# Performance work log

Measured on AMD Instinct MI355X. Metric: run time of the kernel, lower is better.

Reference implementation:

```python
import jax, jax.numpy as jnp
import numpy as np

N_NODES = 100000
N_EDGES = 3200000
N_GRAPHS = 128
IN_DIM = 4
HID = 64
BN_EPS = 1e-5


def setup_inputs() -> dict:
    key = jax.random.key(0)
    ks = jax.random.split(key, 24)
    x = jax.random.normal(ks[0], (N_NODES, IN_DIM), dtype=jnp.float32)
    edge_index = jax.random.randint(ks[1], (2, N_EDGES), 0, N_NODES, dtype=jnp.int32)
    batch_ids = jnp.sort(jax.random.randint(ks[2], (N_NODES,), 0, N_GRAPHS, dtype=jnp.int32))

    def lin(k, out_d, in_d):
        s = 1.0 / np.sqrt(in_d)
        return jax.random.uniform(k, (out_d, in_d), jnp.float32, -s, s)

    inp = {
        'x': x, 'edge_index': edge_index, 'batch_ids': batch_ids,
        # SAGEConv i: out = lin_l(mean_neighbors) + lin_r(x_self); bias lives in lin_l
        'w1l': lin(ks[3], HID, IN_DIM), 'b1': jnp.zeros((HID,), jnp.float32), 'w1r': lin(ks[4], HID, IN_DIM),
        'bn1_g': jnp.ones((HID,), jnp.float32), 'bn1_b': jnp.zeros((HID,), jnp.float32),
        'w2l': lin(ks[5], HID, HID), 'b2': jnp.zeros((HID,), jnp.float32), 'w2r': lin(ks[6], HID, HID),
        'bn2_g': jnp.ones((HID,), jnp.float32), 'bn2_b': jnp.zeros((HID,), jnp.float32),
        'w3l': lin(ks[7], HID, HID), 'b3': jnp.zeros((HID,), jnp.float32), 'w3r': lin(ks[8], HID, HID),
        'bn3_g': jnp.ones((HID,), jnp.float32), 'bn3_b': jnp.zeros((HID,), jnp.float32),
        'fc1_w': lin(ks[9], 64, HID), 'fc1_b': jnp.zeros((64,), jnp.float32),
        'fc2_w': lin(ks[10], 2, 64), 'fc2_b': jnp.zeros((2,), jnp.float32),
    }
    return inp


def _sage(x, src, dst, deg_inv, wl, bl, wr):
    # mean-aggregate neighbor messages (source -> target), then two small GEMMs
    msum = jax.ops.segment_sum(x[src], dst, num_segments=N_NODES)  # [N, d]
    agg = msum * deg_inv[:, None]
    return agg @ wl.T + bl + x @ wr.T


def _bn(x, g, b):
    # BatchNorm1d in training mode: batch stats over node dim, biased variance
    m = jnp.mean(x, axis=0)
    v = jnp.mean((x - m) ** 2, axis=0)
    return (x - m) * jax.lax.rsqrt(v + BN_EPS) * g + b


def reference(x, edge_index, batch_ids,
              w1l, b1, w1r, bn1_g, bn1_b,
              w2l, b2, w2r, bn2_g, bn2_b,
              w3l, b3, w3r, bn3_g, bn3_b,
              fc1_w, fc1_b, fc2_w, fc2_b):
    src, dst = edge_index[0], edge_index[1]
    deg = jax.ops.segment_sum(jnp.ones((src.shape[0],), x.dtype), dst, num_segments=N_NODES)
    deg_inv = 1.0 / jnp.maximum(deg, 1.0)

    h = jax.nn.relu(_bn(_sage(x, src, dst, deg_inv, w1l, b1, w1r), bn1_g, bn1_b))
    h = jax.nn.relu(_bn(_sage(h, src, dst, deg_inv, w2l, b2, w2r), bn2_g, bn2_b))
    h = jax.nn.relu(_bn(_sage(h, src, dst, deg_inv, w3l, b3, w3r), bn3_g, bn3_b))

    # global_mean_pool over graphs
    gsum = jax.ops.segment_sum(h, batch_ids, num_segments=N_GRAPHS)
    gcnt = jax.ops.segment_sum(jnp.ones((h.shape[0],), h.dtype), batch_ids, num_segments=N_GRAPHS)
    pooled = gsum / jnp.maximum(gcnt, 1.0)[:, None]

    # MLP head (dropout = identity at inference)
    hid = jax.nn.relu(pooled @ fc1_w.T + fc1_b)
    return hid @ fc2_w.T + fc2_b
```

## Files before the change

### kernel.cpp

```cpp
#include <hip/hip_runtime.h>
#include <hip/hip_fp16.h>

#define NN 100000
#define NE 3200000
#define NG 128
#define BN_EPS 1e-5f

#define NBUK 782
#define BSHIFT 7
#define BCAP 6144

#define GRID_L1 2048
#define GRID_SG 1024
#define PBMAX 2048

typedef _Float16 h2v __attribute__((ext_vector_type(2)));

__global__ void __launch_bounds__(512) k_scatter(
    const int* __restrict__ src, const int* __restrict__ dst,
    int* __restrict__ slab_cursor, unsigned int* __restrict__ slab, int E) {
    __shared__ int hist[NBUK + 2];
    __shared__ int cbase[NBUK + 2];
    int tid = threadIdx.x;
    int eBeg = blockIdx.x * 6250;
    int eEnd = min(eBeg + 6250, E);

    for (int t = tid; t < NBUK; t += 512) hist[t] = 0;
    __syncthreads();
    for (int e = eBeg + tid; e < eEnd; e += 512) {
        int b = dst[e] >> BSHIFT;
        atomicAdd(&hist[b], 1);
    }
    __syncthreads();
    for (int t = tid; t < NBUK; t += 512) {
        int c = hist[t];
        cbase[t] = (c > 0) ? atomicAdd(&slab_cursor[t], c) : 0;
    }
    __syncthreads();
    for (int t = tid; t < NBUK; t += 512) hist[t] = 0;
    __syncthreads();
    for (int e = eBeg + tid; e < eEnd; e += 512) {
        int d = dst[e];
        int b = d >> BSHIFT;
        int r = atomicAdd(&hist[b], 1);
        int pos = cbase[b] + r;
        if (pos < BCAP) slab[(size_t)b * BCAP + pos] = ((unsigned)src[e] << BSHIFT) | (unsigned)(d & 127);
    }
}

__global__ void k_bucket_scan(const int* __restrict__ slab_cursor,
                              int* __restrict__ bucket_base, int* __restrict__ row_ptr) {
    __shared__ int sm[1024];
    int t = threadIdx.x;
    int c = (t < NBUK) ? min(slab_cursor[t], BCAP) : 0;
    sm[t] = c;
    __syncthreads();
    for (int off = 1; off < 1024; off <<= 1) {
        int add = (t >= off) ? sm[t - off] : 0;
        __syncthreads();
        sm[t] += add;
        __syncthreads();
    }
    if (t < NBUK) {
        bucket_base[t] = sm[t] - c;
        if (t == NBUK - 1) row_ptr[NN] = sm[t];
    }
}

__global__ void __launch_bounds__(512) k_bucket_csr(
    const unsigned int* __restrict__ slab, const int* __restrict__ slab_cursor,
    const int* __restrict__ bucket_base, int* __restrict__ row_ptr,
    float* __restrict__ deg_inv, int* __restrict__ csr_src) {
    __shared__ int sdeg[128];
    __shared__ int sscan[128];
    __shared__ int slcur[128];
    int tid = threadIdx.x;
    int b = blockIdx.x;
    int lo = b << BSHIFT;
    int cnt = min(slab_cursor[b], BCAP);
    const unsigned int* sl = slab + (size_t)b * BCAP;

    if (tid < 128) sdeg[tid] = 0;
    __syncthreads();
    for (int k = tid; k < cnt; k += 512) {
        atomicAdd(&sdeg[sl[k] & 127], 1);
    }
    __syncthreads();
    int v = (tid < 128) ? sdeg[tid] : 0;
    if (tid < 128) sscan[tid] = v;
    __syncthreads();
    for (int off = 1; off < 128; off <<= 1) {
        int add = 0;
        if (tid < 128 && tid >= off) add = sscan[tid - off];
        __syncthreads();
        if (tid < 128) sscan[tid] += add;
        __syncthreads();
    }
    int base = bucket_base[b];
    if (tid < 128) {
        int excl = sscan[tid] - v;
        int n = lo + tid;
        if (n < NN) {
            row_ptr[n] = base + excl;
            deg_inv[n] = 1.0f / fmaxf((float)v, 1.0f);
        }
        slcur[tid] = base + excl;
    }
    __syncthreads();
    for (int k = tid; k < cnt; k += 512) {
        unsigned int p = sl[k];
        int pos = atomicAdd(&slcur[p & 127], 1);
        csr_src[pos] = (int)(p >> BSHIFT);
    }
}

__global__ void __launch_bounds__(256) k_layer1(
    const float* __restrict__ x, const int* __restrict__ row_ptr,
    const int* __restrict__ csr_src, const float* __restrict__ deg_inv,
    const float* __restrict__ w1l, const float* __restrict__ b1,
    const float* __restrict__ w1r, float* __restrict__ h_pre,
    float* __restrict__ part, int N) {
    __shared__ float swl[256], swr[256], sb1[64];
    __shared__ float ssum[64], ssq[64];
    int tid = threadIdx.x;
    swl[tid] = w1l[tid];
    swr[tid] = w1r[tid];
    if (tid < 64) { sb1[tid] = b1[tid]; ssum[tid] = 0.f; ssq[tid] = 0.f; }
    __syncthreads();

    int g = tid & 15, ni = tid >> 4;
    const int ntiles = N / 16;

    for (int tile = blockIdx.x; tile < ntiles; tile += gridDim.x) {
        int n = tile * 16 + ni;
        int r0 = row_ptr[n], r1 = row_ptr[n + 1];
        float4 acc = make_float4(0.f, 0.f, 0.f, 0.f);
        for (int e = r0 + g; e < r1; e += 16) {
            int s = csr_src[e];
            float4 xv = ((const float4*)x)[s];
            acc.x += xv.x; acc.y += xv.y; acc.z += xv.z; acc.w += xv.w;
        }
        for (int m = 1; m < 16; m <<= 1) {
            acc.x += __shfl_xor(acc.x, m);
            acc.y += __shfl_xor(acc.y, m);
            acc.z += __shfl_xor(acc.z, m);
            acc.w += __shfl_xor(acc.w, m);
        }
        float di = deg_inv[n];
        float ax = acc.x * di, ay = acc.y * di, az = acc.z * di, aw = acc.w * di;
        float4 xs = ((const float4*)x)[n];

        float4 o;
        float* op = &o.x;
#pragma unroll
        for (int m = 0; m < 4; m++) {
            int j = 4 * g + m;
            float s = sb1[j];
            s += ax * swl[j * 4 + 0] + ay * swl[j * 4 + 1] + az * swl[j * 4 + 2] + aw * swl[j * 4 + 3];
            s += xs.x * swr[j * 4 + 0] + xs.y * swr[j * 4 + 1] + xs.z * swr[j * 4 + 2] + xs.w * swr[j * 4 + 3];
            op[m] = s;
        }
        ((float4*)h_pre)[n * 16 + g] = o;

        float4 q = make_float4(o.x * o.x, o.y * o.y, o.z * o.z, o.w * o.w);
#pragma unroll
        for (int m = 16; m <= 32; m <<= 1) {
            o.x += __shfl_xor(o.x, m); o.y += __shfl_xor(o.y, m);
            o.z += __shfl_xor(o.z, m); o.w += __shfl_xor(o.w, m);
            q.x += __shfl_xor(q.x, m); q.y += __shfl_xor(q.y, m);
            q.z += __shfl_xor(q.z, m); q.w += __shfl_xor(q.w, m);
        }
        if ((tid & 48) == 0) {
            atomicAdd(&ssum[4 * g + 0], o.x); atomicAdd(&ssum[4 * g + 1], o.y);
            atomicAdd(&ssum[4 * g + 2], o.z); atomicAdd(&ssum[4 * g + 3], o.w);
            atomicAdd(&ssq[4 * g + 0], q.x);  atomicAdd(&ssq[4 * g + 1], q.y);
            atomicAdd(&ssq[4 * g + 2], q.z);  atomicAdd(&ssq[4 * g + 3], q.w);
        }
    }
    __syncthreads();
    if (tid < 64) {
        part[(2 * tid) * PBMAX + blockIdx.x]     = ssum[tid];
        part[(2 * tid + 1) * PBMAX + blockIdx.x] = ssq[tid];
    }
}

__global__ void __launch_bounds__(512, 8) k_sage(
    const __half* __restrict__ h_in, const int* __restrict__ row_ptr,
    const int* __restrict__ csr_src, const float* __restrict__ deg_inv,
    const float* __restrict__ wl, const float* __restrict__ bl,
    const float* __restrict__ wr, float* __restrict__ h_pre,
    float* __restrict__ part) {
    __shared__ h2v wl2s[32][68];
    __shared__ h2v wr2s[32][68];
    __shared__ h2v tAh[32][36];
    __shared__ h2v tXh[32][36];
    __shared__ float ssum[64], ssq[64];
    int tid = threadIdx.x;
    for (int idx = tid; idx < 2048; idx += 512) {
        int j = idx & 63, kk = idx >> 6;
        float2 l = ((const float2*)wl)[j * 32 + kk];
        float2 r = ((const float2*)wr)[j * 32 + kk];
        wl2s[kk][j] = h2v{(_Float16)l.x, (_Float16)l.y};
        wr2s[kk][j] = h2v{(_Float16)r.x, (_Float16)r.y};
    }
    if (tid < 64) { ssum[tid] = 0.f; ssq[tid] = 0.f; }
    __syncthreads();

    int g = tid & 15, ni = tid >> 4;
    const uint2* tbl = (const uint2*)h_in;
    const int ntiles = NN / 32;

    for (int tile = blockIdx.x; tile < ntiles; tile += gridDim.x) {
        int n = tile * 32 + ni;
        float ax = 0.f, ay = 0.f, az = 0.f, aw = 0.f;
        int r0 = row_ptr[n], r1 = row_ptr[n + 1];
        int e = r0;
        for (; e + 4 <= r1; e += 4) {
            int s0 = csr_src[e], s1 = csr_src[e + 1], s2 = csr_src[e + 2], s3 = csr_src[e + 3];
            uint2 v0 = tbl[(size_t)s0 * 16 + g];
            uint2 v1 = tbl[(size_t)s1 * 16 + g];
            uint2 v2 = tbl[(size_t)s2 * 16 + g];
            uint2 v3 = tbl[(size_t)s3 * 16 + g];
            float2 f;
            f = __half22float2(*(__half2*)&v0.x); ax += f.x; ay += f.y;
            f = __half22float2(*(__half2*)&v0.y); az += f.x; aw += f.y;
            f = __half22float2(*(__half2*)&v1.x); ax += f.x; ay += f.y;
            f = __half22float2(*(__half2*)&v1.y); az += f.x; aw += f.y;
            f = __half22float2(*(__half2*)&v2.x); ax += f.x; ay += f.y;
            f = __half22float2(*(__half2*)&v2.y); az += f.x; aw += f.y;
            f = __half22float2(*(__half2*)&v3.x); ax += f.x; ay += f.y;
            f = __half22float2(*(__half2*)&v3.y); az += f.x; aw += f.y;
        }
        for (; e < r1; ++e) {
            int s = csr_src[e];
            uint2 v = tbl[(size_t)s * 16 + g];
            float2 f;
            f = __half22float2(*(__half2*)&v.x); ax += f.x; ay += f.y;
            f = __half22float2(*(__half2*)&v.y); az += f.x; aw += f.y;
        }
        float di = deg_inv[n];
        uint2 rs = tbl[(size_t)n * 16 + g];
        ax *= di; ay *= di; az *= di; aw *= di;
        tAh[ni][2 * g]     = h2v{(_Float16)ax, (_Float16)ay};
        tAh[ni][2 * g + 1] = h2v{(_Float16)az, (_Float16)aw};
        *(uint2*)&tXh[ni][2 * g] = rs;
        __syncthreads();

        float4 o = ((const float4*)bl)[g];
#pragma unroll 4
        for (int kk = 0; kk < 32; kk++) {
            h2v a2 = tAh[ni][kk];
            h2v x2 = tXh[ni][kk];
            h2v l0 = wl2s[kk][4 * g + 0], l1 = wl2s[kk][4 * g + 1];
            h2v l2 = wl2s[kk][4 * g + 2], l3 = wl2s[kk][4 * g + 3];
            h2v r0v = wr2s[kk][4 * g + 0], r1v = wr2s[kk][4 * g + 1];
            h2v r2v = wr2s[kk][4 * g + 2], r3v = wr2s[kk][4 * g + 3];
#if __has_builtin(__builtin_amdgcn_fdot2)
            o.x = __builtin_amdgcn_fdot2(a2, l0, o.x, false);
            o.y = __builtin_amdgcn_fdot2(a2, l1, o.y, false);
            o.z = __builtin_amdgcn_fdot2(a2, l2, o.z, false);
            o.w = __builtin_amdgcn_fdot2(a2, l3, o.w, false);
            o.x = __builtin_amdgcn_fdot2(x2, r0v, o.x, false);
            o.y = __builtin_amdgcn_fdot2(x2, r1v, o.y, false);
            o.z = __builtin_amdgcn_fdot2(x2, r2v, o.z, false);
            o.w = __builtin_amdgcn_fdot2(x2, r3v, o.w, false);
#else
            float a0 = (float)a2.x, a1 = (float)a2.y, x0 = (float)x2.x, x1 = (float)x2.y;
            o.x += a0 * (float)l0.x + a1 * (float)l0.y + x0 * (float)r0v.x + x1 * (float)r0v.y;
            o.y += a0 * (float)l1.x + a1 * (float)l1.y + x0 * (float)r1v.x + x1 * (float)r1v.y;
            o.z += a0 * (float)l2.x + a1 * (float)l2.y + x0 * (float)r2v.x + x1 * (float)r2v.y;
            o.w += a0 * (float)l3.x + a1 * (float)l3.y + x0 * (float)r3v.x + x1 * (float)r3v.y;
#endif
        }
        ((float4*)h_pre)[(size_t)n * 16 + g] = o;

        float4 q = make_float4(o.x * o.x, o.y * o.y, o.z * o.z, o.w * o.w);
#pragma unroll
        for (int m = 16; m <= 32; m <<= 1) {
            o.x += __shfl_xor(o.x, m); o.y += __shfl_xor(o.y, m);
            o.z += __shfl_xor(o.z, m); o.w += __shfl_xor(o.w, m);
            q.x += __shfl_xor(q.x, m); q.y += __shfl_xor(q.y, m);
            q.z += __shfl_xor(q.z, m); q.w += __shfl_xor(q.w, m);
        }
        if ((tid & 48) == 0) {
            atomicAdd(&ssum[4 * g + 0], o.x); atomicAdd(&ssum[4 * g + 1], o.y);
            atomicAdd(&ssum[4 * g + 2], o.z); atomicAdd(&ssum[4 * g + 3], o.w);
            atomicAdd(&ssq[4 * g + 0], q.x);  atomicAdd(&ssq[4 * g + 1], q.y);
            atomicAdd(&ssq[4 * g + 2], q.z);  atomicAdd(&ssq[4 * g + 3], q.w);
        }
        __syncthreads();
    }
    if (tid < 64) {
        part[(2 * tid) * PBMAX + blockIdx.x]     = ssum[tid];
        part[(2 * tid + 1) * PBMAX + blockIdx.x] = ssq[tid];
    }
}

__global__ void k_reduce_sb(const float* __restrict__ part, int PB,
                            const float* __restrict__ gamma, const float* __restrict__ beta,
                            float* __restrict__ sbv, int N) {
    int c = blockIdx.x;
    float s = 0.f, q = 0.f;
    for (int b = threadIdx.x; b < PB; b += 256) {
        s += part[(2 * c) * PBMAX + b];
        q += part[(2 * c + 1) * PBMAX + b];
    }
    __shared__ float rs[256], rq[256];
    rs[threadIdx.x] = s;
    rq[threadIdx.x] = q;
    __syncthreads();
    for (int off = 128; off > 0; off >>= 1) {
        if (threadIdx.x < off) {
            rs[threadIdx.x] += rs[threadIdx.x + off];
            rq[threadIdx.x] += rq[threadIdx.x + off];
        }
        __syncthreads();
    }
    if (threadIdx.x == 0) {
        float m = rs[0] / (float)N;
        float var = rq[0] / (float)N - m * m;
        float sc = gamma[c] * rsqrtf(var + BN_EPS);
        sbv[c]      = sc;
        sbv[64 + c] = beta[c] - m * sc;
    }
}

__global__ void k_bnrelu_h(const float* __restrict__ h_pre, const float* __restrict__ sbv,
                           __half* __restrict__ h, int N) {
    __shared__ float s_sc[64], s_bi[64];
    if (threadIdx.x < 64) {
        s_sc[threadIdx.x] = sbv[threadIdx.x];
        s_bi[threadIdx.x] = sbv[64 + threadIdx.x];
    }
    __syncthreads();
    int total = N * 16;
    for (int i = blockIdx.x * blockDim.x + threadIdx.x; i < total; i += gridDim.x * blockDim.x) {
        float4 v = ((const float4*)h_pre)[i];
        int c4 = (i & 15) * 4;
        v.x = fmaxf(v.x * s_sc[c4 + 0] + s_bi[c4 + 0], 0.f);
        v.y = fmaxf(v.y * s_sc[c4 + 1] + s_bi[c4 + 1], 0.f);
        v.z = fmaxf(v.z * s_sc[c4 + 2] + s_bi[c4 + 2], 0.f);
        v.w = fmaxf(v.w * s_sc[c4 + 3] + s_bi[c4 + 3], 0.f);
        __half2 p0 = __floats2half2_rn(v.x, v.y);
        __half2 p1 = __floats2half2_rn(v.z, v.w);
        uint2 o;
        o.x = *(unsigned int*)&p0;
        o.y = *(unsigned int*)&p1;
        ((uint2*)h)[i] = o;
    }
}

__global__ void k_poolhead(const __half* __restrict__ h, const int* __restrict__ batch,
                           const float* __restrict__ fc1w, const float* __restrict__ fc1b,
                           const float* __restrict__ fc2w, const float* __restrict__ fc2b,
                           float* __restrict__ out, int N) {
    int gph = blockIdx.x;
    int lo = 0, hi = N;
    while (lo < hi) { int mid = (lo + hi) >> 1; if (batch[mid] < gph) lo = mid + 1; else hi = mid; }
    int start = lo;
    hi = N;
    while (lo < hi) { int mid = (lo + hi) >> 1; if (batch[mid] < gph + 1) lo = mid + 1; else hi = mid; }
    int end = lo;

    int c = threadIdx.x & 63, w = threadIdx.x >> 6;
    float s = 0.f;
    for (int r = start + w; r < end; r += 4) s += __half2float(h[r * 64 + c]);
    __shared__ float sm[256];
    __shared__ float pl[64], hid[64];
    sm[threadIdx.x] = s;
    __syncthreads();
    if (threadIdx.x < 64) {
        float t = sm[c] + sm[64 + c] + sm[128 + c] + sm[192 + c];
        pl[c] = t / fmaxf((float)(end - start), 1.0f);
    }
    __syncthreads();
    if (threadIdx.x < 64) {
        int j = threadIdx.x;
        float v = fc1b[j];
        for (int k = 0; k < 64; k++) v += pl[k] * fc1w[j * 64 + k];
        hid[j] = fmaxf(v, 0.f);
    }
    __syncthreads();
    if (threadIdx.x < 2) {
        int j = threadIdx.x;
        float o = fc2b[j];
        for (int k = 0; k < 64; k++) o += hid[k] * fc2w[j * 64 + k];
        out[gph * 2 + j] = o;
    }
}

extern "C" void kernel_launch(void* const* d_in, const int* in_sizes, int n_in,
                              void* d_out, int out_size, void* d_ws, size_t ws_size,
                              hipStream_t stream) {
    const float* x    = (const float*)d_in[0];
    const int* ei     = (const int*)d_in[1];
    const int* batch  = (const int*)d_in[2];
    const float* w1l  = (const float*)d_in[3];
    const float* b1   = (const float*)d_in[4];
    const float* w1r  = (const float*)d_in[5];
    const float* bn1g = (const float*)d_in[6];
    const float* bn1b = (const float*)d_in[7];
    const float* w2l  = (const float*)d_in[8];
    const float* b2   = (const float*)d_in[9];
    const float* w2r  = (const float*)d_in[10];
    const float* bn2g = (const float*)d_in[11];
    const float* bn2b = (const float*)d_in[12];
    const float* w3l  = (const float*)d_in[13];
    const float* b3   = (const float*)d_in[14];
    const float* w3r  = (const float*)d_in[15];
    const float* bn3g = (const float*)d_in[16];
    const float* bn3b = (const float*)d_in[17];
    const float* fc1w = (const float*)d_in[18];
    const float* fc1b = (const float*)d_in[19];
    const float* fc2w = (const float*)d_in[20];
    const float* fc2b = (const float*)d_in[21];
    float* out = (float*)d_out;

    const int N = NN, E = NE;
    const int* srcp = ei;
    const int* dstp = ei + E;

    char* ws = (char*)d_ws;
    size_t off = 0;
    auto alloc = [&](size_t bytes) -> char* {
        char* p = ws + off;
        off += (bytes + 255) & ~(size_t)255;
        return p;
    };
    int* csr_src       = (int*)alloc(sizeof(int) * E);
    float* hB          = (float*)alloc(sizeof(float) * N * 64);
    __half* hH         = (__half*)alloc(sizeof(__half) * N * 64);
    unsigned int* slab = (unsigned int*)alloc(sizeof(unsigned int) * (size_t)NBUK * BCAP);
    int* slab_cursor   = (int*)alloc(sizeof(int) * NBUK);
    int* bucket_base   = (int*)alloc(sizeof(int) * NBUK);
    int* row_ptr       = (int*)alloc(sizeof(int) * (N + 1));
    float* deg_inv     = (float*)alloc(sizeof(float) * N);
    float* part        = (float*)alloc(sizeof(float) * 128 * PBMAX);
    float* sbv         = (float*)alloc(sizeof(float) * 128);

    hipMemsetAsync(slab_cursor, 0, sizeof(int) * NBUK, stream);

    k_scatter<<<512, 512, 0, stream>>>(srcp, dstp, slab_cursor, slab, E);
    k_bucket_scan<<<1, 1024, 0, stream>>>(slab_cursor, bucket_base, row_ptr);
    k_bucket_csr<<<NBUK, 512, 0, stream>>>(slab, slab_cursor, bucket_base, row_ptr, deg_inv, csr_src);

    k_layer1<<<GRID_L1, 256, 0, stream>>>(x, row_ptr, csr_src, deg_inv, w1l, b1, w1r, hB, part, N);
    k_reduce_sb<<<64, 256, 0, stream>>>(part, GRID_L1, bn1g, bn1b, sbv, N);
    k_bnrelu_h<<<1024, 256, 0, stream>>>(hB, sbv, hH, N);

    k_sage<<<GRID_SG, 512, 0, stream>>>(hH, row_ptr, csr_src, deg_inv, w2l, b2, w2r, hB, part);
    k_reduce_sb<<<64, 256, 0, stream>>>(part, GRID_SG, bn2g, bn2b, sbv, N);
    k_bnrelu_h<<<1024, 256, 0, stream>>>(hB, sbv, hH, N);

    k_sage<<<GRID_SG, 512, 0, stream>>>(hH, row_ptr, csr_src, deg_inv, w3l, b3, w3r, hB, part);
    k_reduce_sb<<<64, 256, 0, stream>>>(part, GRID_SG, bn3g, bn3b, sbv, N);
    k_bnrelu_h<<<1024, 256, 0, stream>>>(hB, sbv, hH, N);

    k_poolhead<<<NG, 256, 0, stream>>>(hH, batch, fc1w, fc1b, fc2w, fc2b, out, N);
}
```

Before: 469.3 us.

## Fuse layer-1 SAGE into CSR build and chunk fp16 features by column group

Layer 1's aggregation and linear transform now run inside the bucket CSR kernel. The kernel stages the bucket's CSR in LDS and gathers x directly, so the separate k_layer1 pass and its reread of csr_src go away. The fp16 hidden-feature table changes from row-major 128-byte rows to four column chunks of 32 bytes per node. k_sage then processes one chunk at a time, splitting edges across 4 lanes, to improve cache locality of the random gathers. The costs are more LDS use in the CSR kernel, extra shuffles and passes over csr_src in k_sage, and a matching change to the pooling and BN layouts.

```diff
diff --git a/kernel.cpp b/kernel.cpp
--- a/kernel.cpp
+++ b/kernel.cpp
@@ -10,9 +10,10 @@
 #define BSHIFT 7
 #define BCAP 6144
 
-#define GRID_L1 2048
 #define GRID_SG 1024
 #define PBMAX 2048
+
+#define CHUNK_U2 (NN * 4)
 
 typedef _Float16 h2v __attribute__((ext_vector_type(2)));
 
@@ -70,16 +71,24 @@
 __global__ void __launch_bounds__(512) k_bucket_csr(
     const unsigned int* __restrict__ slab, const int* __restrict__ slab_cursor,
     const int* __restrict__ bucket_base, int* __restrict__ row_ptr,
-    float* __restrict__ deg_inv, int* __restrict__ csr_src) {
+    float* __restrict__ deg_inv, int* __restrict__ csr_src,
+    const float* __restrict__ x, const float* __restrict__ w1l,
+    const float* __restrict__ b1, const float* __restrict__ w1r,
+    float* __restrict__ h_pre, float* __restrict__ part) {
+    __shared__ int lds_csr[BCAP];
     __shared__ int sdeg[128];
     __shared__ int sscan[128];
     __shared__ int slcur[128];
+    __shared__ float swl[256], swr[256], sb1[64];
+    __shared__ float ssum[64], ssq[64];
     int tid = threadIdx.x;
     int b = blockIdx.x;
     int lo = b << BSHIFT;
     int cnt = min(slab_cursor[b], BCAP);
     const unsigned int* sl = slab + (size_t)b * BCAP;
 
+    if (tid < 256) { swl[tid] = w1l[tid]; swr[tid] = w1r[tid]; }
+    if (tid < 64)  { sb1[tid] = b1[tid]; ssum[tid] = 0.f; ssq[tid] = 0.f; }
     if (tid < 128) sdeg[tid] = 0;
     __syncthreads();
     for (int k = tid; k < cnt; k += 512) {
@@ -104,77 +113,69 @@
             row_ptr[n] = base + excl;
             deg_inv[n] = 1.0f / fmaxf((float)v, 1.0f);
         }
-        slcur[tid] = base + excl;
+        slcur[tid] = excl;
     }
     __syncthreads();
     for (int k = tid; k < cnt; k += 512) {
         unsigned int p = sl[k];
         int pos = atomicAdd(&slcur[p & 127], 1);
-        csr_src[pos] = (int)(p >> BSHIFT);
-    }
-}
-
-__global__ void __launch_bounds__(256) k_layer1(
-    const float* __restrict__ x, const int* __restrict__ row_ptr,
-    const int* __restrict__ csr_src, const float* __restrict__ deg_inv,
-    const float* __restrict__ w1l, const float* __restrict__ b1,
-    const float* __restrict__ w1r, float* __restrict__ h_pre,
-    float* __restrict__ part, int N) {
-    __shared__ float swl[256], swr[256], sb1[64];
-    __shared__ float ssum[64], ssq[64];
-    int tid = threadIdx.x;
-    swl[tid] = w1l[tid];
-    swr[tid] = w1r[tid];
-    if (tid < 64) { sb1[tid] = b1[tid]; ssum[tid] = 0.f; ssq[tid] = 0.f; }
-    __syncthreads();
-
-    int g = tid & 15, ni = tid >> 4;
-    const int ntiles = N / 16;
-
-    for (int tile = blockIdx.x; tile < ntiles; tile += gridDim.x) {
-        int n = tile * 16 + ni;
-        int r0 = row_ptr[n], r1 = row_ptr[n + 1];
-        float4 acc = make_float4(0.f, 0.f, 0.f, 0.f);
-        for (int e = r0 + g; e < r1; e += 16) {
-            int s = csr_src[e];
-            float4 xv = ((const float4*)x)[s];
-            acc.x += xv.x; acc.y += xv.y; acc.z += xv.z; acc.w += xv.w;
-        }
-        for (int m = 1; m < 16; m <<= 1) {
-            acc.x += __shfl_xor(acc.x, m);
-            acc.y += __shfl_xor(acc.y, m);
-            acc.z += __shfl_xor(acc.z, m);
-            acc.w += __shfl_xor(acc.w, m);
-        }
-        float di = deg_inv[n];
-        float ax = acc.x * di, ay = acc.y * di, az = acc.z * di, aw = acc.w * di;
-        float4 xs = ((const float4*)x)[n];
-
-        float4 o;
+        lds_csr[pos] = (int)(p >> BSHIFT);
+    }
+    __syncthreads();
+    for (int k = tid; k < cnt; k += 512) csr_src[base + k] = lds_csr[k];
+
+    int i = tid >> 2, c = tid & 3;
+    int n = lo + i;
+    bool valid = (n < NN);
+    int dhi = sscan[i];
+    int dlo = dhi - sdeg[i];
+    const float4* x4 = (const float4*)x;
+    float4 acc = make_float4(0.f, 0.f, 0.f, 0.f);
+    for (int k = dlo + c; k < dhi; k += 4) {
+        int s = lds_csr[k];
+        float4 xv = x4[s];
+        acc.x += xv.x; acc.y += xv.y; acc.z += xv.z; acc.w += xv.w;
+    }
+#pragma unroll
+    for (int m = 1; m <= 2; m <<= 1) {
+        acc.x += __shfl_xor(acc.x, m);
+        acc.y += __shfl_xor(acc.y, m);
+        acc.z += __shfl_xor(acc.z, m);
+        acc.w += __shfl_xor(acc.w, m);
+    }
+    float dv = 1.0f / fmaxf((float)sdeg[i], 1.0f);
+    float ax = acc.x * dv, ay = acc.y * dv, az = acc.z * dv, aw = acc.w * dv;
+    float4 xs = valid ? x4[n] : make_float4(0.f, 0.f, 0.f, 0.f);
+
+#pragma unroll
+    for (int m4 = 0; m4 < 4; m4++) {
+        float4 o = make_float4(0.f, 0.f, 0.f, 0.f);
         float* op = &o.x;
-#pragma unroll
-        for (int m = 0; m < 4; m++) {
-            int j = 4 * g + m;
-            float s = sb1[j];
-            s += ax * swl[j * 4 + 0] + ay * swl[j * 4 + 1] + az * swl[j * 4 + 2] + aw * swl[j * 4 + 3];
-            s += xs.x * swr[j * 4 + 0] + xs.y * swr[j * 4 + 1] + xs.z * swr[j * 4 + 2] + xs.w * swr[j * 4 + 3];
-            op[m] = s;
-        }
-        ((float4*)h_pre)[n * 16 + g] = o;
-
+        if (valid) {
+#pragma unroll
+            for (int t = 0; t < 4; t++) {
+                int j = c * 16 + m4 * 4 + t;
+                float s = sb1[j];
+                s += ax * swl[j * 4 + 0] + ay * swl[j * 4 + 1] + az * swl[j * 4 + 2] + aw * swl[j * 4 + 3];
+                s += xs.x * swr[j * 4 + 0] + xs.y * swr[j * 4 + 1] + xs.z * swr[j * 4 + 2] + xs.w * swr[j * 4 + 3];
+                op[t] = s;
+            }
+            ((float4*)h_pre)[(size_t)n * 16 + c * 4 + m4] = o;
+        }
         float4 q = make_float4(o.x * o.x, o.y * o.y, o.z * o.z, o.w * o.w);
 #pragma unroll
-        for (int m = 16; m <= 32; m <<= 1) {
+        for (int m = 4; m <= 32; m <<= 1) {
             o.x += __shfl_xor(o.x, m); o.y += __shfl_xor(o.y, m);
             o.z += __shfl_xor(o.z, m); o.w += __shfl_xor(o.w, m);
             q.x += __shfl_xor(q.x, m); q.y += __shfl_xor(q.y, m);
             q.z += __shfl_xor(q.z, m); q.w += __shfl_xor(q.w, m);
         }
-        if ((tid & 48) == 0) {
-            atomicAdd(&ssum[4 * g + 0], o.x); atomicAdd(&ssum[4 * g + 1], o.y);
-            atomicAdd(&ssum[4 * g + 2], o.z); atomicAdd(&ssum[4 * g + 3], o.w);
-            atomicAdd(&ssq[4 * g + 0], q.x);  atomicAdd(&ssq[4 * g + 1], q.y);
-            atomicAdd(&ssq[4 * g + 2], q.z);  atomicAdd(&ssq[4 * g + 3], q.w);
+        if ((tid & 63) < 4) {
+            int jb = c * 16 + m4 * 4;
+            atomicAdd(&ssum[jb + 0], o.x); atomicAdd(&ssum[jb + 1], o.y);
+            atomicAdd(&ssum[jb + 2], o.z); atomicAdd(&ssum[jb + 3], o.w);
+            atomicAdd(&ssq[jb + 0], q.x);  atomicAdd(&ssq[jb + 1], q.y);
+            atomicAdd(&ssq[jb + 2], q.z);  atomicAdd(&ssq[jb + 3], q.w);
         }
     }
     __syncthreads();
@@ -207,43 +208,57 @@
     __syncthreads();
 
     int g = tid & 15, ni = tid >> 4;
+    int q = g & 3, eo = g >> 2;
     const uint2* tbl = (const uint2*)h_in;
     const int ntiles = NN / 32;
 
     for (int tile = blockIdx.x; tile < ntiles; tile += gridDim.x) {
         int n = tile * 32 + ni;
-        float ax = 0.f, ay = 0.f, az = 0.f, aw = 0.f;
         int r0 = row_ptr[n], r1 = row_ptr[n + 1];
-        int e = r0;
-        for (; e + 4 <= r1; e += 4) {
-            int s0 = csr_src[e], s1 = csr_src[e + 1], s2 = csr_src[e + 2], s3 = csr_src[e + 3];
-            uint2 v0 = tbl[(size_t)s0 * 16 + g];
-            uint2 v1 = tbl[(size_t)s1 * 16 + g];
-            uint2 v2 = tbl[(size_t)s2 * 16 + g];
-            uint2 v3 = tbl[(size_t)s3 * 16 + g];
-            float2 f;
-            f = __half22float2(*(__half2*)&v0.x); ax += f.x; ay += f.y;
-            f = __half22float2(*(__half2*)&v0.y); az += f.x; aw += f.y;
-            f = __half22float2(*(__half2*)&v1.x); ax += f.x; ay += f.y;
-            f = __half22float2(*(__half2*)&v1.y); az += f.x; aw += f.y;
-            f = __half22float2(*(__half2*)&v2.x); ax += f.x; ay += f.y;
-            f = __half22float2(*(__half2*)&v2.y); az += f.x; aw += f.y;
-            f = __half22float2(*(__half2*)&v3.x); ax += f.x; ay += f.y;
-            f = __half22float2(*(__half2*)&v3.y); az += f.x; aw += f.y;
-        }
-        for (; e < r1; ++e) {
-            int s = csr_src[e];
-            uint2 v = tbl[(size_t)s * 16 + g];
-            float2 f;
-            f = __half22float2(*(__half2*)&v.x); ax += f.x; ay += f.y;
-            f = __half22float2(*(__half2*)&v.y); az += f.x; aw += f.y;
-        }
         float di = deg_inv[n];
-        uint2 rs = tbl[(size_t)n * 16 + g];
-        ax *= di; ay *= di; az *= di; aw *= di;
-        tAh[ni][2 * g]     = h2v{(_Float16)ax, (_Float16)ay};
-        tAh[ni][2 * g + 1] = h2v{(_Float16)az, (_Float16)aw};
-        *(uint2*)&tXh[ni][2 * g] = rs;
+#pragma unroll
+        for (int ch = 0; ch < 4; ch++) {
+            const uint2* cb = tbl + (size_t)ch * CHUNK_U2;
+            float a0 = 0.f, a1 = 0.f, a2 = 0.f, a3 = 0.f;
+            int e = r0 + eo;
+            for (; e + 12 < r1; e += 16) {
+                int s0 = csr_src[e], s1 = csr_src[e + 4], s2 = csr_src[e + 8], s3 = csr_src[e + 12];
+                uint2 v0 = cb[s0 * 4 + q];
+                uint2 v1 = cb[s1 * 4 + q];
+                uint2 v2 = cb[s2 * 4 + q];
+                uint2 v3 = cb[s3 * 4 + q];
+                float2 f;
+                f = __half22float2(*(__half2*)&v0.x); a0 += f.x; a1 += f.y;
+                f = __half22float2(*(__half2*)&v0.y); a2 += f.x; a3 += f.y;
+                f = __half22float2(*(__half2*)&v1.x); a0 += f.x; a1 += f.y;
+                f = __half22float2(*(__half2*)&v1.y); a2 += f.x; a3 += f.y;
+                f = __half22float2(*(__half2*)&v2.x); a0 += f.x; a1 += f.y;
+                f = __half22float2(*(__half2*)&v2.y); a2 += f.x; a3 += f.y;
+                f = __half22float2(*(__half2*)&v3.x); a0 += f.x; a1 += f.y;
+                f = __half22float2(*(__half2*)&v3.y); a2 += f.x; a3 += f.y;
+            }
+            for (; e < r1; e += 4) {
+                int s = csr_src[e];
+                uint2 v = cb[s * 4 + q];
+                float2 f;
+                f = __half22float2(*(__half2*)&v.x); a0 += f.x; a1 += f.y;
+                f = __half22float2(*(__half2*)&v.y); a2 += f.x; a3 += f.y;
+            }
+#pragma unroll
+            for (int m = 4; m <= 8; m <<= 1) {
+                a0 += __shfl_xor(a0, m);
+                a1 += __shfl_xor(a1, m);
+                a2 += __shfl_xor(a2, m);
+                a3 += __shfl_xor(a3, m);
+            }
+            if (eo == 0) {
+                uint2 rs = cb[n * 4 + q];
+                a0 *= di; a1 *= di; a2 *= di; a3 *= di;
+                tAh[ni][ch * 8 + q * 2]     = h2v{(_Float16)a0, (_Float16)a1};
+                tAh[ni][ch * 8 + q * 2 + 1] = h2v{(_Float16)a2, (_Float16)a3};
+                *(uint2*)&tXh[ni][ch * 8 + q * 2] = rs;
+            }
+        }
         __syncthreads();
 
         float4 o = ((const float4*)bl)[g];
@@ -265,28 +280,28 @@
             o.z = __builtin_amdgcn_fdot2(x2, r2v, o.z, false);
             o.w = __builtin_amdgcn_fdot2(x2, r3v, o.w, false);
 #else
-            float a0 = (float)a2.x, a1 = (float)a2.y, x0 = (float)x2.x, x1 = (float)x2.y;
-            o.x += a0 * (float)l0.x + a1 * (float)l0.y + x0 * (float)r0v.x + x1 * (float)r0v.y;
-            o.y += a0 * (float)l1.x + a1 * (float)l1.y + x0 * (float)r1v.x + x1 * (float)r1v.y;
-            o.z += a0 * (float)l2.x + a1 * (float)l2.y + x0 * (float)r2v.x + x1 * (float)r2v.y;
-            o.w += a0 * (float)l3.x + a1 * (float)l3.y + x0 * (float)r3v.x + x1 * (float)r3v.y;
+            float b0 = (float)a2.x, b1 = (float)a2.y, x0 = (float)x2.x, x1 = (float)x2.y;
+            o.x += b0 * (float)l0.x + b1 * (float)l0.y + x0 * (float)r0v.x + x1 * (float)r0v.y;
+            o.y += b0 * (float)l1.x + b1 * (float)l1.y + x0 * (float)r1v.x + x1 * (float)r1v.y;
+            o.z += b0 * (float)l2.x + b1 * (float)l2.y + x0 * (float)r2v.x + x1 * (float)r2v.y;
+            o.w += b0 * (float)l3.x + b1 * (float)l3.y + x0 * (float)r3v.x + x1 * (float)r3v.y;
 #endif
         }
         ((float4*)h_pre)[(size_t)n * 16 + g] = o;
 
-        float4 q = make_float4(o.x * o.x, o.y * o.y, o.z * o.z, o.w * o.w);
+        float4 qv = make_float4(o.x * o.x, o.y * o.y, o.z * o.z, o.w * o.w);
 #pragma unroll
         for (int m = 16; m <= 32; m <<= 1) {
             o.x += __shfl_xor(o.x, m); o.y += __shfl_xor(o.y, m);
             o.z += __shfl_xor(o.z, m); o.w += __shfl_xor(o.w, m);
-            q.x += __shfl_xor(q.x, m); q.y += __shfl_xor(q.y, m);
-            q.z += __shfl_xor(q.z, m); q.w += __shfl_xor(q.w, m);
+            qv.x += __shfl_xor(qv.x, m); qv.y += __shfl_xor(qv.y, m);
+            qv.z += __shfl_xor(qv.z, m); qv.w += __shfl_xor(qv.w, m);
         }
         if ((tid & 48) == 0) {
             atomicAdd(&ssum[4 * g + 0], o.x); atomicAdd(&ssum[4 * g + 1], o.y);
             atomicAdd(&ssum[4 * g + 2], o.z); atomicAdd(&ssum[4 * g + 3], o.w);
-            atomicAdd(&ssq[4 * g + 0], q.x);  atomicAdd(&ssq[4 * g + 1], q.y);
-            atomicAdd(&ssq[4 * g + 2], q.z);  atomicAdd(&ssq[4 * g + 3], q.w);
+            atomicAdd(&ssq[4 * g + 0], qv.x);  atomicAdd(&ssq[4 * g + 1], qv.y);
+            atomicAdd(&ssq[4 * g + 2], qv.z);  atomicAdd(&ssq[4 * g + 3], qv.w);
         }
         __syncthreads();
     }
@@ -336,7 +351,9 @@
     int total = N * 16;
     for (int i = blockIdx.x * blockDim.x + threadIdx.x; i < total; i += gridDim.x * blockDim.x) {
         float4 v = ((const float4*)h_pre)[i];
-        int c4 = (i & 15) * 4;
+        int g = i & 15;
+        int n = i >> 4;
+        int c4 = g * 4;
         v.x = fmaxf(v.x * s_sc[c4 + 0] + s_bi[c4 + 0], 0.f);
         v.y = fmaxf(v.y * s_sc[c4 + 1] + s_bi[c4 + 1], 0.f);
         v.z = fmaxf(v.z * s_sc[c4 + 2] + s_bi[c4 + 2], 0.f);
@@ -346,7 +363,7 @@
         uint2 o;
         o.x = *(unsigned int*)&p0;
         o.y = *(unsigned int*)&p1;
-        ((uint2*)h)[i] = o;
+        ((uint2*)h)[(size_t)(g >> 2) * CHUNK_U2 + n * 4 + (g & 3)] = o;
     }
 }
 
@@ -363,8 +380,9 @@
     int end = lo;
 
     int c = threadIdx.x & 63, w = threadIdx.x >> 6;
+    size_t cbase = (size_t)(c >> 4) * (NN * 16) + (c & 15);
     float s = 0.f;
-    for (int r = start + w; r < end; r += 4) s += __half2float(h[r * 64 + c]);
+    for (int r = start + w; r < end; r += 4) s += __half2float(h[cbase + (size_t)r * 16]);
     __shared__ float sm[256];
     __shared__ float pl[64], hid[64];
     sm[threadIdx.x] = s;
@@ -442,10 +460,9 @@
 
     k_scatter<<<512, 512, 0, stream>>>(srcp, dstp, slab_cursor, slab, E);
     k_bucket_scan<<<1, 1024, 0, stream>>>(slab_cursor, bucket_base, row_ptr);
-    k_bucket_csr<<<NBUK, 512, 0, stream>>>(slab, slab_cursor, bucket_base, row_ptr, deg_inv, csr_src);
-
-    k_layer1<<<GRID_L1, 256, 0, stream>>>(x, row_ptr, csr_src, deg_inv, w1l, b1, w1r, hB, part, N);
-    k_reduce_sb<<<64, 256, 0, stream>>>(part, GRID_L1, bn1g, bn1b, sbv, N);
+    k_bucket_csr<<<NBUK, 512, 0, stream>>>(slab, slab_cursor, bucket_base, row_ptr, deg_inv,
+                                           csr_src, x, w1l, b1, w1r, hB, part);
+    k_reduce_sb<<<64, 256, 0, stream>>>(part, NBUK, bn1g, bn1b, sbv, N);
     k_bnrelu_h<<<1024, 256, 0, stream>>>(hB, sbv, hH, N);
 
     k_sage<<<GRID_SG, 512, 0, stream>>>(hH, row_ptr, csr_src, deg_inv, w2l, b2, w2r, hB, part);
```

After: 614.7 us. 1.31x slower.
